# Kernel optimization log

Measured on AMD Instinct MI355X. Metric: run time of the kernel, lower is better.

The kernel has to match this reference:

```python
import jax, jax.numpy as jnp
import numpy as np

B, H, HD, E = 4, 32, 128, 4096
PAST = 2048
SB = int(0.1 * PAST)   # start_budget fixed at prefill
RB = int(0.1 * PAST)   # recent_budget fixed at prefill
MERGE = 32             # merge_budget inside local_cam_mask


def setup_inputs() -> dict:
    key = jax.random.key(0)
    ks = jax.random.split(key, 10)
    S = PAST + 1
    # attention_masks_next built at the previous decode step:
    # ones on sink tokens [0:SB+1] and the trailing recent window [PAST-RB:S]
    m = jnp.zeros((B * H, S), jnp.float32)
    m = m.at[:, :SB + 1].set(1.0)
    m = m.at[:, PAST - RB:].set(1.0)
    w = lambda k: jax.random.normal(k, (E, E), jnp.float32) * 0.02
    return {
        "hidden_states": jax.random.normal(ks[0], (B, 1, E), jnp.float32),
        "past_key": jax.random.normal(ks[1], (B, H, PAST, HD), jnp.float32),
        "past_value": jax.random.normal(ks[2], (B, H, PAST, HD), jnp.float32),
        "attention_mask": jnp.zeros((B, 1, 1, S), jnp.float32),
        "attn_masks_next": m[:, None, :],
        "previous_scores": jax.random.uniform(ks[3], (B * H, PAST), jnp.float32, 0.0, 2.0),
        "Wq": w(ks[4]), "bq": jnp.zeros((E,), jnp.float32),
        "Wk": w(ks[5]), "bk": jnp.zeros((E,), jnp.float32),
        "Wv": w(ks[6]), "bv": jnp.zeros((E,), jnp.float32),
        "Wo": w(ks[7]), "bo": jnp.zeros((E,), jnp.float32),
        "start_budget": SB,
        "recent_budget": RB,
    }


def reference(hidden_states, past_key, past_value, attention_mask, attn_masks_next,
              previous_scores, Wq, bq, Wk, bk, Wv, bv, Wo, bo,
              start_budget, recent_budget):
    B_, T, E_ = hidden_states.shape
    H_, hd = past_key.shape[1], past_key.shape[-1]
    scaling = hd ** -0.5
    # projections (torch Linear: x @ W^T + b); q pre-scaled as in the module
    q = (hidden_states @ Wq.T + bq) * scaling
    k_new = (hidden_states @ Wk.T + bk).reshape(B_, T, H_, hd).transpose(0, 2, 1, 3)
    v_new = (hidden_states @ Wv.T + bv).reshape(B_, T, H_, hd).transpose(0, 2, 1, 3)
    k = jnp.concatenate([past_key, k_new], axis=2)   # [B,H,S,hd]
    v = jnp.concatenate([past_value, v_new], axis=2)
    S = k.shape[2]
    q = q.reshape(B_, T, H_, hd).transpose(0, 2, 1, 3).reshape(B_ * H_, T, hd)
    k = k.reshape(B_ * H_, S, hd)
    v = v.reshape(B_ * H_, S, hd)
    aw = jnp.einsum('bth,bsh->bts', q, k)            # [B*H, T, S]
    fmin = jnp.finfo(aw.dtype).min
    aw = aw.reshape(B_, H_, T, S) + attention_mask
    aw = jnp.maximum(aw, fmin).reshape(B_ * H_, T, S)
    # CAM eviction mask from the previous step
    aw = aw * attn_masks_next + (1.0 - attn_masks_next) * fmin
    # local_cam_mask: merge the evicted token's value into the next MERGE slots
    ti = previous_scores.shape[-1]                   # == S-1
    mean_attn = jnp.mean(jnp.concatenate(
        [previous_scores[:, :start_budget], previous_scores[:, ti - recent_budget:ti]],
        axis=-1), axis=-1)                            # [B*H]
    merge_prob = previous_scores[:, ti - recent_budget] / mean_attn
    merge_mask = (merge_prob > 1.0).astype(v.dtype)
    score1 = v[:, ti - recent_budget, :] * merge_mask[:, None] / MERGE  # [B*H,hd]
    v = v.at[:, ti - recent_budget + 1: ti - recent_budget + MERGE + 1, :].add(score1[:, None, :])
    v = v.at[:, start_budget, :].multiply(0.99)
    aw = jax.nn.softmax(aw, axis=-1)
    # decode step (previous_scores is not None): pin the merge-sink column to 1
    aw = aw.at[:, :, start_budget].set(1.0)
    out = jnp.einsum('bts,bsh->bth', aw, v)          # [B*H, T, hd]
    out = out.reshape(B_, H_, T, hd).transpose(0, 2, 1, 3).reshape(B_, T, E_)
    return out @ Wo.T + bo
```

## Files before the change

### kernel.cpp

```cpp
#include <hip/hip_runtime.h>
#include <cstdint>
#include <cstddef>

#define FMIN_F (-3.402823466e38f)

__device__ __forceinline__ float wave_sum(float v) {
#pragma unroll
    for (int off = 32; off > 0; off >>= 1)
        v += __shfl_down(v, off, 64);
    return v;
}

template <int NMAT>
__global__ __launch_bounds__(256) void gemv_wide_kernel(
    const float* __restrict__ X,
    const float* __restrict__ W0, const float* __restrict__ W1,
    const float* __restrict__ W2,
    float* __restrict__ part)
{
    const int wave = threadIdx.x >> 6;
    const int lane = threadIdx.x & 63;

    int bid = blockIdx.x;
    const int mi = (NMAT == 1) ? 0 : (bid >> 10);
    bid &= 1023;
    const int s    = bid & 7;
    const int quad = bid >> 3;
    const int r0   = quad * 32 + wave * 8;
    const int k0q  = s * 128;
    const int lo   = k0q + lane * 2;

    const float* W = (mi == 0) ? W0 : (mi == 1) ? W1 : W2;
    const float4* W4 = (const float4*)W;
    const float4* X4 = (const float4*)X;

    float4 xv[4][2];
#pragma unroll
    for (int b = 0; b < 4; ++b)
#pragma unroll
        for (int j = 0; j < 2; ++j)
            xv[b][j] = X4[b * 1024 + lo + j];

    float acc[8][4];
#pragma unroll
    for (int r = 0; r < 8; ++r)
#pragma unroll
        for (int b = 0; b < 4; ++b) acc[r][b] = 0.f;

#pragma unroll
    for (int g = 0; g < 2; ++g) {
        float4 w[4][2];
#pragma unroll
        for (int rr = 0; rr < 4; ++rr)
#pragma unroll
            for (int j = 0; j < 2; ++j)
                w[rr][j] = W4[(size_t)(r0 + g * 4 + rr) * 1024 + lo + j];
#pragma unroll
        for (int rr = 0; rr < 4; ++rr)
#pragma unroll
            for (int j = 0; j < 2; ++j)
#pragma unroll
                for (int b = 0; b < 4; ++b)
                    acc[g * 4 + rr][b] += w[rr][j].x * xv[b][j].x
                                        + w[rr][j].y * xv[b][j].y
                                        + w[rr][j].z * xv[b][j].z
                                        + w[rr][j].w * xv[b][j].w;
    }

#pragma unroll
    for (int r = 0; r < 8; ++r)
#pragma unroll
        for (int b = 0; b < 4; ++b) {
            float v = wave_sum(acc[r][b]);
            if (lane == 0)
                part[(((size_t)mi * 8 + s) * 4 + b) * 4096 + (r0 + r)] = v;
        }
}

__global__ __launch_bounds__(256) void gemv_reduce_kernel(
    const float* __restrict__ part,
    const float* __restrict__ B0, const float* __restrict__ B1,
    const float* __restrict__ B2,
    float scale0,
    float* __restrict__ Y)
{
    const int idx = blockIdx.x * 256 + threadIdx.x;
    const int mi = idx >> 14;
    const int b  = (idx >> 12) & 3;
    const int r  = idx & 4095;
    float s = 0.f;
#pragma unroll
    for (int k = 0; k < 8; ++k)
        s += part[(((size_t)mi * 8 + k) * 4 + b) * 4096 + r];
    const float* Bs = (mi == 0) ? B0 : (mi == 1) ? B1 : B2;
    s += Bs[r];
    if (mi == 0) s *= scale0;
    Y[((size_t)(mi * 4 + b)) * 4096 + r] = s;
}

__global__ __launch_bounds__(256) void score_kernel(
    const float* __restrict__ qkv,
    const float* __restrict__ pk,
    const float* __restrict__ amask,
    const float* __restrict__ cam,
    const int* __restrict__ sbp, const int* __restrict__ rbp,
    float* __restrict__ scores)
{
    constexpr int PAST = 2048, S = 2049, HD = 128;
    const int bh = blockIdx.y;
    const int b  = bh >> 5;
    const int h  = bh & 31;
    const int SB = sbp[0], RB = rbp[0];
    const int NS = SB + 1;
    const int NA = NS + RB + 1;

    const int wave = threadIdx.x >> 6;
    const int lane = threadIdx.x & 63;

    const float* qh   = qkv + (size_t)b * 4096 + h * HD;
    const float* knew = qkv + (size_t)(4 + b) * 4096 + h * HD;
    const float2 ql = ((const float2*)qh)[lane];

#pragma unroll
    for (int j = 0; j < 8; ++j) {
        const int i = blockIdx.x * 32 + j * 4 + wave;
        if (i >= NA) continue;
        const int s = (i < NS) ? i : (PAST - RB + (i - NS));
        const float2* kr = (s < PAST)
            ? (const float2*)(pk + ((size_t)bh * PAST + s) * HD)
            : (const float2*)knew;
        const float2 kk = kr[lane];
        float p = ql.x * kk.x + ql.y * kk.y;
        p = wave_sum(p);
        if (lane == 0) {
            const float m  = cam[(size_t)bh * S + s];
            float sc = fmaxf(p + amask[(size_t)b * S + s], FMIN_F);
            sc = sc * m + (1.0f - m) * FMIN_F;
            scores[(size_t)bh * 512 + i] = sc;
        }
    }
}

__global__ __launch_bounds__(256) void softmax_kernel(
    const float* __restrict__ ps,
    const int* __restrict__ sbp, const int* __restrict__ rbp,
    float* __restrict__ scores)
{
    constexpr int PAST = 2048;
    const int bh = blockIdx.x;
    const int SB = sbp[0], RB = rbp[0];
    const int NS = SB + 1;
    const int NA = NS + RB + 1;
    const int tid = threadIdx.x;

    __shared__ float s_c[512];
    __shared__ float s_red[256];
    __shared__ float s_mm;

    for (int i = tid; i < NA; i += 256) s_c[i] = scores[(size_t)bh * 512 + i];

    {
        float part = 0.0f;
        const int cnt = SB + RB;
        for (int i = tid; i < cnt; i += 256) {
            const int idx = (i < SB) ? i : (PAST - RB + (i - SB));
            part += ps[(size_t)bh * PAST + idx];
        }
        s_red[tid] = part;
    }
    __syncthreads();
#pragma unroll
    for (int st = 128; st > 0; st >>= 1) {
        if (tid < st) s_red[tid] += s_red[tid + st];
        __syncthreads();
    }
    if (tid == 0) {
        const float mean = s_red[0] / (float)(SB + RB);
        const float prob = ps[(size_t)bh * PAST + (PAST - RB)] / mean;
        s_mm = (prob > 1.0f) ? (1.0f / 32.0f) : 0.0f;
    }
    __syncthreads();

    float mx = -INFINITY;
    for (int i = tid; i < NA; i += 256) mx = fmaxf(mx, s_c[i]);
    s_red[tid] = mx;
    __syncthreads();
#pragma unroll
    for (int st = 128; st > 0; st >>= 1) {
        if (tid < st) s_red[tid] = fmaxf(s_red[tid], s_red[tid + st]);
        __syncthreads();
    }
    const float gmax = s_red[0];
    __syncthreads();

    float lsum = 0.0f;
    for (int i = tid; i < NA; i += 256) {
        const float e = expf(s_c[i] - gmax);
        s_c[i] = e;
        lsum += e;
    }
    s_red[tid] = lsum;
    __syncthreads();
#pragma unroll
    for (int st = 128; st > 0; st >>= 1) {
        if (tid < st) s_red[tid] += s_red[tid + st];
        __syncthreads();
    }
    const float inv = 1.0f / s_red[0];
    __syncthreads();
    for (int i = tid; i < NA; i += 256) s_c[i] *= inv;
    __syncthreads();

    if (tid == 0) {
        float sm = 0.0f;
#pragma unroll
        for (int j = 1; j <= 32; ++j) sm += s_c[NS + j];
        s_c[NS] += s_mm * sm;
        s_c[SB]  = 0.99f;
    }
    __syncthreads();

    for (int i = tid; i < NA; i += 256) scores[(size_t)bh * 512 + i] = s_c[i];
}

__global__ __launch_bounds__(256) void pv_kernel(
    const float* __restrict__ qkv,
    const float* __restrict__ pv,
    const float* __restrict__ coeff,
    const int* __restrict__ sbp, const int* __restrict__ rbp,
    float* __restrict__ partial)
{
    constexpr int PAST = 2048, HD = 128;
    const int bh = blockIdx.y;
    const int b  = bh >> 5;
    const int h  = bh & 31;
    const int SB = sbp[0], RB = rbp[0];
    const int NS = SB + 1;
    const int NA = NS + RB + 1;
    const int CPC = (NA + 7) >> 3;
    const int i0 = blockIdx.x * CPC;
    const int i1 = min(NA, i0 + CPC);

    const int tid  = threadIdx.x;
    const int d    = tid & 127;
    const int half = tid >> 7;

    __shared__ float s_co[64];
    __shared__ float s_red[256];

    if (tid < i1 - i0) s_co[tid] = coeff[(size_t)bh * 512 + i0 + tid];
    __syncthreads();

    const float* vnew = qkv + (size_t)(8 + b) * 4096 + h * HD;

    float acc = 0.0f;
    for (int i = i0 + half; i < i1; i += 2) {
        const int s = (i < NS) ? i : (PAST - RB + (i - NS));
        const float* vr = (s < PAST)
            ? (pv + ((size_t)bh * PAST + s) * HD)
            : vnew;
        acc += s_co[i - i0] * vr[d];
    }
    s_red[tid] = acc;
    __syncthreads();
    if (tid < 128)
        partial[((size_t)bh * 8 + blockIdx.x) * HD + d] = s_red[tid] + s_red[tid + 128];
}

__global__ __launch_bounds__(256) void attn_reduce_kernel(
    const float* __restrict__ partial,
    float* __restrict__ attn_out)
{
    const int idx = blockIdx.x * 256 + threadIdx.x;
    const int bh = idx >> 7;
    const int d  = idx & 127;
    float s = 0.0f;
#pragma unroll
    for (int c = 0; c < 8; ++c)
        s += partial[(size_t)bh * 1024 + c * 128 + d];
    attn_out[idx] = s;
}

extern "C" void kernel_launch(void* const* d_in, const int* in_sizes, int n_in,
                              void* d_out, int out_size, void* d_ws, size_t ws_size,
                              hipStream_t stream)
{
    const float* hs = (const float*)d_in[0];
    const float* pk = (const float*)d_in[1];
    const float* pv = (const float*)d_in[2];
    const float* am = (const float*)d_in[3];
    const float* cm = (const float*)d_in[4];
    const float* ps = (const float*)d_in[5];
    const float* Wq = (const float*)d_in[6];
    const float* bq = (const float*)d_in[7];
    const float* Wk = (const float*)d_in[8];
    const float* bk = (const float*)d_in[9];
    const float* Wv = (const float*)d_in[10];
    const float* bv = (const float*)d_in[11];
    const float* Wo = (const float*)d_in[12];
    const float* bo = (const float*)d_in[13];
    const int*   sb = (const int*)d_in[14];
    const int*   rb = (const int*)d_in[15];

    float* qkv   = (float*)d_ws;
    float* aout  = qkv + 3 * 4 * 4096;
    float* sc    = aout + 4 * 4096;
    float* part  = sc + 128 * 512;
    float* gpart = part + 128 * 8 * 128;
    float* out   = (float*)d_out;

    const float scaling = 0.08838834764831845f;

    gemv_wide_kernel<3><<<3072, 256, 0, stream>>>(hs, Wq, Wk, Wv, gpart);
    gemv_reduce_kernel<<<192, 256, 0, stream>>>(gpart, bq, bk, bv, scaling, qkv);

    score_kernel<<<dim3(16, 128), 256, 0, stream>>>(qkv, pk, am, cm, sb, rb, sc);
    softmax_kernel<<<128, 256, 0, stream>>>(ps, sb, rb, sc);
    pv_kernel<<<dim3(8, 128), 256, 0, stream>>>(qkv, pv, sc, sb, rb, part);
    attn_reduce_kernel<<<64, 256, 0, stream>>>(part, aout);

    gemv_wide_kernel<1><<<1024, 256, 0, stream>>>(aout, Wo, Wo, Wo, gpart);
    gemv_reduce_kernel<<<64, 256, 0, stream>>>(gpart, bo, bo, bo, 1.0f, out);
}
```

Measured before the change: 111.2 us.

## Restructure GEMV to stage activations in LDS with two K-slices

```diff
diff --git a/kernel.cpp b/kernel.cpp
--- a/kernel.cpp
+++ b/kernel.cpp
@@ -12,68 +12,64 @@
 }
 
 template <int NMAT>
-__global__ __launch_bounds__(256) void gemv_wide_kernel(
+__global__ __launch_bounds__(256, 4) void gemv_fused_kernel(
     const float* __restrict__ X,
     const float* __restrict__ W0, const float* __restrict__ W1,
     const float* __restrict__ W2,
     float* __restrict__ part)
 {
-    const int wave = threadIdx.x >> 6;
-    const int lane = threadIdx.x & 63;
-
+    __shared__ float4 sX[4][512];
+    const int tid = threadIdx.x;
     int bid = blockIdx.x;
-    const int mi = (NMAT == 1) ? 0 : (bid >> 10);
-    bid &= 1023;
-    const int s    = bid & 7;
-    const int quad = bid >> 3;
-    const int r0   = quad * 32 + wave * 8;
-    const int k0q  = s * 128;
-    const int lo   = k0q + lane * 2;
-
+    const int mi    = (NMAT == 1) ? 0 : (bid >> 9);
+    const int rem   = (NMAT == 1) ? bid : (bid & 511);
+    const int slice = rem & 1;
+    const int r0    = (rem >> 1) * 16;
+    const int ko    = slice * 512;
+
+    const float4* X4 = (const float4*)X;
+    for (int i = tid; i < 2048; i += 256) {
+        const int b = i >> 9, j = i & 511;
+        sX[b][j] = X4[b * 1024 + ko + j];
+    }
+    __syncthreads();
+
+    const int wave = tid >> 6;
+    const int lane = tid & 63;
     const float* W = (mi == 0) ? W0 : (mi == 1) ? W1 : W2;
     const float4* W4 = (const float4*)W;
-    const float4* X4 = (const float4*)X;
-
-    float4 xv[4][2];
-#pragma unroll
-    for (int b = 0; b < 4; ++b)
-#pragma unroll
-        for (int j = 0; j < 2; ++j)
-            xv[b][j] = X4[b * 1024 + lo + j];
-
-    float acc[8][4];
-#pragma unroll
-    for (int r = 0; r < 8; ++r)
+    const int rbase = r0 + wave * 4;
+
+    float acc[4][4];
+#pragma unroll
+    for (int r = 0; r < 4; ++r)
 #pragma unroll
         for (int b = 0; b < 4; ++b) acc[r][b] = 0.f;
 
 #pragma unroll
-    for (int g = 0; g < 2; ++g) {
-        float4 w[4][2];
-#pragma unroll
-        for (int rr = 0; rr < 4; ++rr)
-#pragma unroll
-            for (int j = 0; j < 2; ++j)
-                w[rr][j] = W4[(size_t)(r0 + g * 4 + rr) * 1024 + lo + j];
-#pragma unroll
-        for (int rr = 0; rr < 4; ++rr)
-#pragma unroll
-            for (int j = 0; j < 2; ++j)
-#pragma unroll
-                for (int b = 0; b < 4; ++b)
-                    acc[g * 4 + rr][b] += w[rr][j].x * xv[b][j].x
-                                        + w[rr][j].y * xv[b][j].y
-                                        + w[rr][j].z * xv[b][j].z
-                                        + w[rr][j].w * xv[b][j].w;
-    }
-
-#pragma unroll
-    for (int r = 0; r < 8; ++r)
+    for (int row = 0; row < 4; ++row) {
+        const float4* Wr = W4 + (size_t)(rbase + row) * 1024 + ko;
+        float4 w[8];
+#pragma unroll
+        for (int u = 0; u < 8; ++u) w[u] = Wr[u * 64 + lane];
+#pragma unroll
+        for (int u = 0; u < 8; ++u) {
+#pragma unroll
+            for (int b = 0; b < 4; ++b) {
+                const float4 x = sX[b][u * 64 + lane];
+                acc[row][b] += w[u].x * x.x + w[u].y * x.y
+                             + w[u].z * x.z + w[u].w * x.w;
+            }
+        }
+    }
+
+#pragma unroll
+    for (int row = 0; row < 4; ++row)
 #pragma unroll
         for (int b = 0; b < 4; ++b) {
-            float v = wave_sum(acc[r][b]);
+            float v = wave_sum(acc[row][b]);
             if (lane == 0)
-                part[(((size_t)mi * 8 + s) * 4 + b) * 4096 + (r0 + r)] = v;
+                part[(((size_t)mi * 2 + slice) * 4 + b) * 4096 + (rbase + row)] = v;
         }
 }
 
@@ -88,10 +84,8 @@
     const int mi = idx >> 14;
     const int b  = (idx >> 12) & 3;
     const int r  = idx & 4095;
-    float s = 0.f;
-#pragma unroll
-    for (int k = 0; k < 8; ++k)
-        s += part[(((size_t)mi * 8 + k) * 4 + b) * 4096 + r];
+    float s = part[(((size_t)mi * 2 + 0) * 4 + b) * 4096 + r]
+            + part[(((size_t)mi * 2 + 1) * 4 + b) * 4096 + r];
     const float* Bs = (mi == 0) ? B0 : (mi == 1) ? B1 : B2;
     s += Bs[r];
     if (mi == 0) s *= scale0;
@@ -311,7 +305,7 @@
 
     const float scaling = 0.08838834764831845f;
 
-    gemv_wide_kernel<3><<<3072, 256, 0, stream>>>(hs, Wq, Wk, Wv, gpart);
+    gemv_fused_kernel<3><<<1536, 256, 0, stream>>>(hs, Wq, Wk, Wv, gpart);
     gemv_reduce_kernel<<<192, 256, 0, stream>>>(gpart, bq, bk, bv, scaling, qkv);
 
     score_kernel<<<dim3(16, 128), 256, 0, stream>>>(qkv, pk, am, cm, sb, rb, sc);
@@ -319,6 +313,6 @@
     pv_kernel<<<dim3(8, 128), 256, 0, stream>>>(qkv, pv, sc, sb, rb, part);
     attn_reduce_kernel<<<64, 256, 0, stream>>>(part, aout);
 
-    gemv_wide_kernel<1><<<1024, 256, 0, stream>>>(aout, Wo, Wo, Wo, gpart);
+    gemv_fused_kernel<1><<<512, 256, 0, stream>>>(aout, Wo, Wo, Wo, gpart);
     gemv_reduce_kernel<<<64, 256, 0, stream>>>(gpart, bo, bo, bo, 1.0f, out);
 }
```

Result: slower. 289.1 us (+160.1%).
